# Kernel tuning notes

Hardware: AMD Instinct MI355X
Metric: run time of the kernel (lower is better)

## Reference

```python
import jax, jax.numpy as jnp
import numpy as np

N = 50000      # nodes per type
E = 800000     # edges per relation
CIN = 64       # in_channels
H, O = 2, 32   # heads, out_channels
HID = H * O    # hidden
EC = 16        # edge_channels


def setup_inputs() -> dict:
    key = jax.random.key(0)
    ks = jax.random.split(key, 30)
    f = lambda i, shape, s=0.1: jax.random.normal(ks[i], shape, dtype=jnp.float32) * s
    inp = {
        'x_a': f(0, (N, CIN), 1.0), 'x_b': f(1, (N, CIN), 1.0),
        'edge_attr1': f(2, (E, EC), 1.0), 'edge_attr2': f(3, (E, EC), 1.0),
        'Wq_a': f(4, (CIN, HID)), 'Wk_a': f(5, (CIN, HID)), 'Wv_a': f(6, (CIN, HID)),
        'Wq_b': f(7, (CIN, HID)), 'Wk_b': f(8, (CIN, HID)), 'Wv_b': f(9, (CIN, HID)),
        'emb_a': f(10, (HID,)), 'emb_b': f(11, (HID,)),
        'rel1': f(12, (HID,)), 'rel2': f(13, (HID,)),
        'We': f(14, (EC, HID)), 'a_attn': f(15, (4 * O,)),
        'Wo_a': f(16, (HID, O)), 'bo_a': f(17, (O,)),
        'Wo_b': f(18, (HID, O)), 'bo_b': f(19, (O,)),
        'Wr_a': f(20, (CIN, O)), 'Wr_b': f(21, (CIN, O)),
        'row1': jax.random.randint(ks[22], (E,), 0, N),
        'col1': jax.random.randint(ks[23], (E,), 0, N),
        'row2': jax.random.randint(ks[24], (E,), 0, N),
        'col2': jax.random.randint(ks[25], (E,), 0, N),
    }
    return inp


def _edge_softmax(scores, col, num_dst):
    # softmax over incoming edges of each destination node; scores: [E, H]
    m = jax.ops.segment_max(scores, col, num_segments=num_dst)      # [N, H]
    ex = jnp.exp(scores - m[col])
    s = jax.ops.segment_sum(ex, col, num_segments=num_dst)          # [N, H]
    return ex / s[col]


def _relation(q_dst, k_src, v_src, emb_src, emb_dst, rel_emb, edge_bias,
              row, col, a_attn, num_dst):
    eb = edge_bias                                                  # [E, H, O]
    qd = q_dst[col] + emb_dst.reshape(1, H, O)
    ks = k_src[row] + emb_src.reshape(1, H, O)
    rb = jnp.broadcast_to(rel_emb.reshape(1, H, O), qd.shape)
    attn_in = jnp.concatenate([qd, ks, rb, eb], axis=-1)            # [E, H, 4O]
    scores = jnp.einsum('ehd,d->eh', jnp.tanh(attn_in), a_attn)    # [E, H]
    w = _edge_softmax(scores, col, num_dst)                         # [E, H]
    msg = v_src[row] + rel_emb.reshape(1, H, O) + eb                # [E, H, O]
    agg = jax.ops.segment_sum(msg * w[..., None], col, num_segments=num_dst)
    return agg.reshape(num_dst, H * O)


def reference(x_a, x_b, edge_attr1, edge_attr2,
              Wq_a, Wk_a, Wv_a, Wq_b, Wk_b, Wv_b,
              emb_a, emb_b, rel1, rel2, We, a_attn,
              Wo_a, bo_a, Wo_b, bo_b, Wr_a, Wr_b,
              row1, col1, row2, col2):
    q_a = (x_a @ Wq_a).reshape(-1, H, O)
    k_a = (x_a @ Wk_a).reshape(-1, H, O)
    v_a = (x_a @ Wv_a).reshape(-1, H, O)
    q_b = (x_b @ Wq_b).reshape(-1, H, O)
    k_b = (x_b @ Wk_b).reshape(-1, H, O)
    v_b = (x_b @ Wv_b).reshape(-1, H, O)

    # relation r1: a -> b
    eb1 = (edge_attr1 @ We).reshape(-1, H, O)
    out_b = _relation(q_b, k_a, v_a, emb_a, emb_b, rel1, eb1, row1, col1, a_attn, N)
    # relation r2: b -> a
    eb2 = (edge_attr2 @ We).reshape(-1, H, O)
    out_a = _relation(q_a, k_b, v_b, emb_b, emb_a, rel2, eb2, row2, col2, a_attn, N)

    fin_a = out_a @ Wo_a + bo_a + x_a @ Wr_a                        # [N, O]
    fin_b = out_b @ Wo_b + bo_b + x_b @ Wr_b                        # [N, O]
    return jnp.concatenate([fin_a, fin_b], axis=0)                  # [2N, O]
```

## Files before the change

### kernel.cpp

```cpp
#include <hip/hip_runtime.h>
#include <hip/hip_bf16.h>

typedef __hip_bfloat16 bf16;
typedef __attribute__((ext_vector_type(8))) short short8;
typedef __attribute__((ext_vector_type(4))) float float4v;

static __device__ __forceinline__ float b2f(bf16 x) { return __bfloat162float(x); }

static __device__ __forceinline__ float ldf(const void* p, size_t i, int f32) {
    return f32 ? ((const float*)p)[i] : b2f(((const bf16*)p)[i]);
}
static __device__ __forceinline__ void stf(void* p, size_t i, int f32, float v) {
    if (f32) ((float*)p)[i] = v;
    else     ((bf16*)p)[i] = __float2bfloat16(v);
}
static __device__ __forceinline__ unsigned short f2bf_bits(float f) {
    bf16 h = __float2bfloat16(f);
    return *(unsigned short*)&h;
}

static __device__ __forceinline__ float fast_tanh(float x) {
    float t = __expf(2.f * x);
    return 1.f - 2.f * __builtin_amdgcn_rcpf(t + 1.f);
}

__global__ void detect_kernel(const unsigned short* __restrict__ a, int* __restrict__ flag)
{
    __shared__ int cnt;
    if (threadIdx.x == 0) cnt = 0;
    __syncthreads();
    unsigned e = (a[threadIdx.x] >> 7) & 0xFF;
    if (e < 100 || e > 133) atomicAdd(&cnt, 1);
    __syncthreads();
    if (threadIdx.x == 0) *flag = (cnt >= 16) ? 1 : 0;
}

__global__ __launch_bounds__(256) void prep_small_kernel(
    const void* __restrict__ W0, const void* __restrict__ W1,
    const void* __restrict__ W2, const void* __restrict__ W3,
    const void* __restrict__ W4, const void* __restrict__ W5,
    const void* __restrict__ Wr_a, const void* __restrict__ Wr_b,
    const void* __restrict__ We,
    const void* __restrict__ Wo_a, const void* __restrict__ Wo_b,
    const void* __restrict__ rel1, const void* __restrict__ rel2,
    const void* __restrict__ a_attn, const int* __restrict__ flagp,
    unsigned short* __restrict__ wt,
    float* __restrict__ M1, float* __restrict__ c321,
    float* __restrict__ M2, float* __restrict__ c322,
    float* __restrict__ cvals)
{
    const int f32 = *flagp;
    const int bid = blockIdx.x;
    if (bid < 6) {
        const void* src;
        switch (bid) {
            case 0: src = W0; break; case 1: src = W1; break; case 2: src = W2; break;
            case 3: src = W3; break; case 4: src = W4; break; default: src = W5; break;
        }
        unsigned short* dst = wt + bid * 4096;
        for (int i = threadIdx.x; i < 4096; i += 256) {
            int c = i >> 6, j = i & 63;
            dst[j * 64 + c] = f2bf_bits(ldf(src, c * 64 + j, f32));
        }
    } else if (bid < 8) {
        const void* src = (bid == 6) ? Wr_a : Wr_b;
        unsigned short* dst = wt + 24576 + (bid - 6) * 2048;
        for (int i = threadIdx.x; i < 2048; i += 256) {
            int c = i >> 5, j = i & 31;
            dst[j * 64 + c] = f2bf_bits(ldf(src, c * 32 + j, f32));
        }
    } else if (bid < 10) {
        const int sel = bid - 8;
        const void* Wo  = sel ? Wo_a : Wo_b;
        const void* rel = sel ? rel2 : rel1;
        float* M   = sel ? M2 : M1;
        float* c32 = sel ? c322 : c321;
        const int t = threadIdx.x;
        for (int i = t; i < 1024; i += 256) {
            int m = i >> 5, j = i & 31;
            int h = m >> 4, c = m & 15;
            float s = 0.f;
            for (int jj = 0; jj < 32; ++jj)
                s += ldf(We, c * 64 + h * 32 + jj, f32) * ldf(Wo, (size_t)(h * 32 + jj) * 32 + j, f32);
            M[m * 32 + j] = s;
        }
        if (t < 32) {
            float s2 = 0.f;
            for (int ch = 0; ch < 64; ++ch)
                s2 += ldf(rel, ch, f32) * ldf(Wo, (size_t)ch * 32 + t, f32);
            c32[t] = s2;
        }
        if (t == 252 || t == 253) {
            int h = t - 252;
            float s3 = 0.f;
            for (int l = 0; l < 32; ++l)
                s3 += tanhf(ldf(rel, h * 32 + l, f32)) * ldf(a_attn, 64 + l, f32);
            cvals[sel * 2 + h] = s3;
        }
    } else {
        unsigned short* wet = wt + 28672;
        for (int i = threadIdx.x; i < 1024; i += 256) {
            int n = i >> 4, k = i & 15;
            wet[n * 16 + k] = f2bf_bits(ldf(We, k * 64 + n, f32));
        }
    }
}

__global__ __launch_bounds__(256) void node_prep_mfma_kernel(
    const void* __restrict__ x_a, const void* __restrict__ x_b,
    const unsigned short* __restrict__ wt,
    const void* __restrict__ emb_a, const void* __restrict__ emb_b,
    const void* __restrict__ a_attn, const int* __restrict__ flagp,
    unsigned short* __restrict__ v_a, unsigned short* __restrict__ v_b,
    float* __restrict__ r_a, float* __restrict__ r_b,
    float* __restrict__ sq_a, float* __restrict__ sk_a,
    float* __restrict__ sq_b, float* __restrict__ sk_b,
    int n_nodes, int tiles)
{
    const int f32 = *flagp;
    const int wave_id = blockIdx.x * 4 + (threadIdx.x >> 6);
    if (wave_id >= 2 * tiles) return;
    const int type = (wave_id >= tiles);
    const int tile = type ? (wave_id - tiles) : wave_id;

    const void* xp = type ? x_b : x_a;
    const unsigned short* wq = wt + (type ? 3 * 4096 : 0);
    const unsigned short* wk = wq + 4096;
    const unsigned short* wv = wk + 4096;
    const unsigned short* wr = wt + 24576 + (type ? 2048 : 0);
    const void* embp = type ? emb_b : emb_a;
    unsigned short* v_out = type ? v_b : v_a;
    float*  r_out  = type ? r_b : r_a;
    float2* sq_out = (float2*)(type ? sq_b : sq_a);
    float2* sk_out = (float2*)(type ? sk_b : sk_a);

    const int lane = threadIdx.x & 63;
    const int ml   = lane & 15;
    const int g    = lane >> 4;
    const int g8   = g * 8;

    float embc[4], acq[4], ack[4];
    #pragma unroll
    for (int t = 0; t < 4; ++t) {
        int colt = t * 16 + ml;
        embc[t] = ldf(embp, colt, f32);
        acq[t]  = ldf(a_attn, colt & 31, f32);
        ack[t]  = ldf(a_attn, 32 + (colt & 31), f32);
    }

    short8 Bq[4][2], Bk[4][2], Bv[4][2], Br[2][2];
    #pragma unroll
    for (int t = 0; t < 4; ++t) {
        const int rowo = (t * 16 + ml) * 64;
        #pragma unroll
        for (int kh = 0; kh < 2; ++kh) {
            const int o = rowo + kh * 32 + g8;
            Bq[t][kh] = __builtin_bit_cast(short8, *(const uint4*)(wq + o));
            Bk[t][kh] = __builtin_bit_cast(short8, *(const uint4*)(wk + o));
            Bv[t][kh] = __builtin_bit_cast(short8, *(const uint4*)(wv + o));
            if (t < 2)
                Br[t][kh] = __builtin_bit_cast(short8, *(const uint4*)(wr + o));
        }
    }

    const int n0 = tile << 4;
    int nr = n0 + ml; if (nr > n_nodes - 1) nr = n_nodes - 1;
    short8 A0, A1;
    if (f32) {
        const float4* xr = (const float4*)((const float*)xp + (size_t)nr * 64);
        float4 f0 = xr[2*g], f1 = xr[2*g+1], f2 = xr[8+2*g], f3 = xr[9+2*g];
        short8 a0, a1;
        a0[0]=(short)f2bf_bits(f0.x); a0[1]=(short)f2bf_bits(f0.y);
        a0[2]=(short)f2bf_bits(f0.z); a0[3]=(short)f2bf_bits(f0.w);
        a0[4]=(short)f2bf_bits(f1.x); a0[5]=(short)f2bf_bits(f1.y);
        a0[6]=(short)f2bf_bits(f1.z); a0[7]=(short)f2bf_bits(f1.w);
        a1[0]=(short)f2bf_bits(f2.x); a1[1]=(short)f2bf_bits(f2.y);
        a1[2]=(short)f2bf_bits(f2.z); a1[3]=(short)f2bf_bits(f2.w);
        a1[4]=(short)f2bf_bits(f3.x); a1[5]=(short)f2bf_bits(f3.y);
        a1[6]=(short)f2bf_bits(f3.z); a1[7]=(short)f2bf_bits(f3.w);
        A0 = a0; A1 = a1;
    } else {
        const uint4* xr = (const uint4*)((const bf16*)xp + (size_t)nr * 64);
        A0 = __builtin_bit_cast(short8, xr[g]);
        A1 = __builtin_bit_cast(short8, xr[4 + g]);
    }

    float4v accq[4], acck[4], accv[4], accr[2];
    #pragma unroll
    for (int t = 0; t < 4; ++t) {
        float4v z = {0.f, 0.f, 0.f, 0.f};
        accq[t] = z; acck[t] = z; accv[t] = z;
        if (t < 2) accr[t] = z;
    }
    #pragma unroll
    for (int t = 0; t < 4; ++t) {
        accq[t] = __builtin_amdgcn_mfma_f32_16x16x32_bf16(A0, Bq[t][0], accq[t], 0, 0, 0);
        accq[t] = __builtin_amdgcn_mfma_f32_16x16x32_bf16(A1, Bq[t][1], accq[t], 0, 0, 0);
        acck[t] = __builtin_amdgcn_mfma_f32_16x16x32_bf16(A0, Bk[t][0], acck[t], 0, 0, 0);
        acck[t] = __builtin_amdgcn_mfma_f32_16x16x32_bf16(A1, Bk[t][1], acck[t], 0, 0, 0);
        accv[t] = __builtin_amdgcn_mfma_f32_16x16x32_bf16(A0, Bv[t][0], accv[t], 0, 0, 0);
        accv[t] = __builtin_amdgcn_mfma_f32_16x16x32_bf16(A1, Bv[t][1], accv[t], 0, 0, 0);
        if (t < 2) {
            accr[t] = __builtin_amdgcn_mfma_f32_16x16x32_bf16(A0, Br[t][0], accr[t], 0, 0, 0);
            accr[t] = __builtin_amdgcn_mfma_f32_16x16x32_bf16(A1, Br[t][1], accr[t], 0, 0, 0);
        }
    }

    #pragma unroll
    for (int t = 0; t < 4; ++t) {
        #pragma unroll
        for (int r = 0; r < 4; ++r) {
            int node = n0 + g * 4 + r;
            if (node < n_nodes) {
                v_out[(size_t)node * 64 + t * 16 + ml] = f2bf_bits(accv[t][r]);
                if (t < 2) r_out[(size_t)node * 32 + t * 16 + ml] = accr[t][r];
            }
        }
    }

    #pragma unroll
    for (int r = 0; r < 4; ++r) {
        float q0 = fast_tanh(accq[0][r] + embc[0]) * acq[0]
                 + fast_tanh(accq[1][r] + embc[1]) * acq[1];
        float q1 = fast_tanh(accq[2][r] + embc[2]) * acq[2]
                 + fast_tanh(accq[3][r] + embc[3]) * acq[3];
        float k0 = fast_tanh(acck[0][r] + embc[0]) * ack[0]
                 + fast_tanh(acck[1][r] + embc[1]) * ack[1];
        float k1 = fast_tanh(acck[2][r] + embc[2]) * ack[2]
                 + fast_tanh(acck[3][r] + embc[3]) * ack[3];
        #pragma unroll
        for (int o = 1; o < 16; o <<= 1) {
            q0 += __shfl_xor(q0, o, 64); q1 += __shfl_xor(q1, o, 64);
            k0 += __shfl_xor(k0, o, 64); k1 += __shfl_xor(k1, o, 64);
        }
        int node = n0 + g * 4 + r;
        if (ml == 0 && node < n_nodes) {
            sq_out[node] = make_float2(q0, q1);
            sk_out[node] = make_float2(k0, k1);
        }
    }
}

__global__ __launch_bounds__(256) void hist_kernel(
    const int* __restrict__ col1, const int* __restrict__ col2,
    int* __restrict__ cnt, int n_nodes, int num_e)
{
    const int sel = blockIdx.x & 1;
    const int bx  = blockIdx.x >> 1;
    const int* col = sel ? col2 : col1;
    const int rb = sel ? n_nodes : 0;
    int e = bx * 256 + threadIdx.x;
    if (e < num_e) atomicAdd(&cnt[rb + col[e]], 1);
}

__global__ __launch_bounds__(256) void scan1_kernel(const int* __restrict__ cnt,
                                                    int* __restrict__ partial, int n)
{
    __shared__ int wsum[4];
    int t = threadIdx.x;
    int i0 = blockIdx.x * 512 + 2 * t;
    int s = ((i0 < n) ? cnt[i0] : 0) + ((i0 + 1 < n) ? cnt[i0 + 1] : 0);
    #pragma unroll
    for (int o = 32; o; o >>= 1) s += __shfl_xor(s, o, 64);
    if ((t & 63) == 0) wsum[t >> 6] = s;
    __syncthreads();
    if (t == 0) partial[blockIdx.x] = wsum[0] + wsum[1] + wsum[2] + wsum[3];
}

__global__ void scan2_kernel(const int* __restrict__ partial, int* __restrict__ pp,
                             int* __restrict__ off, int nch, int noff)
{
    int lane = threadIdx.x;
    int running = 0;
    for (int base = 0; base < nch; base += 64) {
        int i = base + lane;
        int o = (i < nch) ? partial[i] : 0;
        int v = o;
        #pragma unroll
        for (int d = 1; d < 64; d <<= 1) {
            int u = __shfl_up(v, d, 64);
            if (lane >= d) v += u;
        }
        if (i < nch) pp[i] = running + v - o;
        running += __shfl(v, 63, 64);
    }
    if (lane == 0) off[noff] = running;
}

__global__ __launch_bounds__(256) void scan3_kernel(const int* __restrict__ cnt,
                                                    const int* __restrict__ pp,
                                                    int* __restrict__ off,
                                                    int* __restrict__ cursor, int n)
{
    __shared__ int tmp[256];
    int t = threadIdx.x;
    int i0 = blockIdx.x * 512 + 2 * t;
    int v0 = (i0 < n) ? cnt[i0] : 0;
    int v1 = (i0 + 1 < n) ? cnt[i0 + 1] : 0;
    int pair = v0 + v1;
    tmp[t] = pair;
    __syncthreads();
    for (int d = 1; d < 256; d <<= 1) {
        int x = (t >= d) ? tmp[t - d] : 0;
        __syncthreads();
        tmp[t] += x;
        __syncthreads();
    }
    int excl = tmp[t] - pair + pp[blockIdx.x];
    if (i0 < n)     { off[i0] = excl;          cursor[i0] = excl; }
    if (i0 + 1 < n) { off[i0 + 1] = excl + v0; cursor[i0 + 1] = excl + v0; }
}

__global__ __launch_bounds__(256) void edge_score_scatter_kernel(
    const void* __restrict__ ea1p, const void* __restrict__ ea2p,
    const unsigned short* __restrict__ wet,
    const int* __restrict__ row1, const int* __restrict__ col1,
    const int* __restrict__ row2, const int* __restrict__ col2,
    const float* __restrict__ sq_bp, const float* __restrict__ sk_ap,
    const float* __restrict__ sq_ap, const float* __restrict__ sk_bp,
    const float* __restrict__ cvals, const void* __restrict__ a_attn,
    const int* __restrict__ flagp, int* __restrict__ cursor,
    uint4* __restrict__ payload, int n_nodes, int num_e)
{
    const int f32 = *flagp;
    const int sel = blockIdx.x & 1;
    const int bx  = blockIdx.x >> 1;
    const void* ea = sel ? ea2p : ea1p;
    const int* row = sel ? row2 : row1;
    const int* col = sel ? col2 : col1;
    const float* sq_dst = sel ? sq_ap : sq_bp;
    const float* sk_src = sel ? sk_bp : sk_ap;
    const int rb = sel ? n_nodes : 0;

    const int lane = threadIdx.x & 63;
    const int wv   = threadIdx.x >> 6;
    const int ml   = lane & 15;
    const int g    = lane >> 4;
    const int rsel = lane & 3;

    const int base = bx * 512 + wv * 128;
    if (base >= num_e) return;

    const short8 zero8 = {0, 0, 0, 0, 0, 0, 0, 0};

    short8 B[4];
    #pragma unroll
    for (int t = 0; t < 4; ++t)
        B[t] = (g < 2) ? __builtin_bit_cast(short8, *(const uint4*)(wet + (t * 16 + ml) * 16 + g * 8))
                       : zero8;
    float av[4];
    #pragma unroll
    for (int t = 0; t < 4; ++t) av[t] = ldf(a_attn, 96 + ((t * 16 + ml) & 31), f32);
    const float c0 = cvals[sel * 2 + 0];
    const float c1 = cvals[sel * 2 + 1];

    short8 A[8];
    #pragma unroll
    for (int it = 0; it < 8; ++it) {
        int ec = base + it * 16 + ml; if (ec > num_e - 1) ec = num_e - 1;
        if (g < 2) {
            if (f32) {
                const float4* p = (const float4*)((const float*)ea + (size_t)ec * 16 + g * 8);
                float4 f0 = p[0], f1 = p[1];
                short8 a;
                a[0] = (short)f2bf_bits(f0.x); a[1] = (short)f2bf_bits(f0.y);
                a[2] = (short)f2bf_bits(f0.z); a[3] = (short)f2bf_bits(f0.w);
                a[4] = (short)f2bf_bits(f1.x); a[5] = (short)f2bf_bits(f1.y);
                a[6] = (short)f2bf_bits(f1.z); a[7] = (short)f2bf_bits(f1.w);
                A[it] = a;
            } else {
                A[it] = __builtin_bit_cast(short8, *(const uint4*)((const bf16*)ea + (size_t)ec * 16 + g * 8));
            }
        } else {
            A[it] = zero8;
        }
    }

    int ppos[8]; unsigned psrc[8]; float2 psq[8], psk[8];
    #pragma unroll
    for (int it = 0; it < 8; ++it) {
        ppos[it] = 0; psrc[it] = 0;
        psq[it] = make_float2(0.f, 0.f); psk[it] = make_float2(0.f, 0.f);
    }
    if (ml < 4) {
        int pcol[8];
        #pragma unroll
        for (int it = 0; it < 8; ++it) {
            int e = base + it * 16 + g * 4 + rsel;
            int ec = (e < num_e) ? e : (num_e - 1);
            pcol[it] = col[ec];
            psrc[it] = (unsigned)row[ec];
        }
        #pragma unroll
        for (int it = 0; it < 8; ++it) {
            psq[it] = ((const float2*)sq_dst)[pcol[it]];
            psk[it] = ((const float2*)sk_src)[psrc[it]];
        }
        #pragma unroll
        for (int it = 0; it < 8; ++it) {
            int e = base + it * 16 + g * 4 + rsel;
            ppos[it] = (e < num_e) ? atomicAdd(&cursor[rb + pcol[it]], 1) : 0;
        }
    }

    #pragma unroll
    for (int it = 0; it < 8; ++it) {
        const int e0 = base + it * 16;
        if (e0 < num_e) {
            float4v z = {0.f, 0.f, 0.f, 0.f};
            float4v acc0 = z, acc1 = z, acc2 = z, acc3 = z;
            acc0 = __builtin_amdgcn_mfma_f32_16x16x32_bf16(A[it], B[0], acc0, 0, 0, 0);
            acc1 = __builtin_amdgcn_mfma_f32_16x16x32_bf16(A[it], B[1], acc1, 0, 0, 0);
            acc2 = __builtin_amdgcn_mfma_f32_16x16x32_bf16(A[it], B[2], acc2, 0, 0, 0);
            acc3 = __builtin_amdgcn_mfma_f32_16x16x32_bf16(A[it], B[3], acc3, 0, 0, 0);

            float s0[4], s1[4];
            #pragma unroll
            for (int r = 0; r < 4; ++r) {
                s0[r] = fast_tanh(acc0[r]) * av[0] + fast_tanh(acc1[r]) * av[1];
                s1[r] = fast_tanh(acc2[r]) * av[2] + fast_tanh(acc3[r]) * av[3];
            }
            #pragma unroll
            for (int o = 1; o < 16; o <<= 1) {
                #pragma unroll
                for (int r = 0; r < 4; ++r) {
                    s0[r] += __shfl_xor(s0[r], o, 64);
                    s1[r] += __shfl_xor(s1[r], o, 64);
                }
            }

            const bool fin = (ml < 4) && (e0 + g * 4 + rsel < num_e);
            if (fin) {
                float a0 = (rsel == 0) ? s0[0] : (rsel == 1) ? s0[1] : (rsel == 2) ? s0[2] : s0[3];
                float a1 = (rsel == 0) ? s1[0] : (rsel == 1) ? s1[1] : (rsel == 2) ? s1[2] : s1[3];
                float v0 = fminf(30.f, fmaxf(-30.f, a0 + psq[it].x + psk[it].x + c0));
                float v1 = fminf(30.f, fmaxf(-30.f, a1 + psq[it].y + psk[it].y + c1));
                uint4* rec = payload + (size_t)3 * ppos[it];
                rec[0] = make_uint4(psrc[it], __float_as_uint(__expf(v0)),
                                    __float_as_uint(__expf(v1)), 0u);
            }
            const int srcl = ((lane & 12) << 2) | (lane & 3);
            const int posx = __shfl(ppos[it], srcl, 64);
            if (lane < 32 && (e0 + ml < num_e)) {
                uint4* rec = payload + (size_t)3 * posx;
                rec[1 + g] = __builtin_bit_cast(uint4, A[it]);
            }
        }
    }
}

__global__ __launch_bounds__(256) void agg_final_kernel(
    const uint4* __restrict__ payload, const int* __restrict__ off,
    const unsigned short* __restrict__ v_a, const unsigned short* __restrict__ v_b,
    const float* __restrict__ r_a, const float* __restrict__ r_b,
    const void* __restrict__ Wo_a, const void* __restrict__ Wo_b,
    const void* __restrict__ bo_a, const void* __restrict__ bo_b,
    const float* __restrict__ M1, const float* __restrict__ M2,
    const float* __restrict__ c321, const float* __restrict__ c322,
    const int* __restrict__ flagp, void* __restrict__ out,
    int n_nodes, int nbh)
{
    const int sel = blockIdx.x & 1;
    const int bx  = blockIdx.x >> 1;
    const unsigned short* v_src = sel ? v_b : v_a;
    const float* r_src = sel ? r_a : r_b;
    const void*  Wo    = sel ? Wo_a : Wo_b;
    const void*  bo    = sel ? bo_a : bo_b;
    const float* M     = sel ? M2 : M1;
    const float* c32   = sel ? c322 : c321;
    const int relbase  = sel ? n_nodes : 0;
    const size_t out_off = sel ? 0 : (size_t)n_nodes * 32;

    const int f32  = *flagp;
    const int lane = threadIdx.x & 63;
    const int wv   = threadIdx.x >> 6;
    const int j    = lane & 31;
    const int half = lane >> 5;
    const int c16  = lane & 15;
    const bool hi  = (lane >= 32);

    __shared__ float stage[4][96];

    float WoR[32], MR[16];
    const int cb = half * 32;
    #pragma unroll
    for (int cc = 0; cc < 32; ++cc)
        WoR[cc] = ldf(Wo, (size_t)(cb + cc) * 32 + j, f32);
    const int ub = half * 16;
    #pragma unroll
    for (int cc = 0; cc < 16; ++cc) MR[cc] = M[(ub + cc) * 32 + j];
    const float boR  = ldf(bo, j, f32);
    const float c32R = c32[j];

    const int stride = nbh * 4;
    const int iters  = (n_nodes + stride - 1) / stride;
    int d = bx * 4 + wv;

    for (int it = 0; it < iters; ++it, d += stride) {
        const bool valid = (d < n_nodes);
        const int dd  = valid ? d : (n_nodes - 1);
        const int idx = relbase + dd;
        const int b   = __builtin_amdgcn_readfirstlane(off[idx]);
        const int en  = __builtin_amdgcn_readfirstlane(off[idx + 1]);
        const int deg = en - b;

        const float rv = r_src[(size_t)dd * 32 + j];

        float den0 = 0.f, den1 = 0.f, y = 0.f, ua = 0.f;
        int k = b;
        #pragma unroll 1
        for (; k + 8 <= en; k += 8) {
            uint4 m[8];
            #pragma unroll
            for (int q = 0; q < 8; ++q) m[q] = payload[(size_t)3 * (k + q)];
            float ev[8];
            #pragma unroll
            for (int q = 0; q < 8; ++q) {
                const unsigned short* pq = (const unsigned short*)(payload + (size_t)3 * (k + q) + 1);
                ev[q] = __uint_as_float((unsigned)pq[c16] << 16);
            }
            float vv[8];
            #pragma unroll
            for (int q = 0; q < 8; ++q)
                vv[q] = __uint_as_float((unsigned)v_src[(size_t)m[q].x * 64 + lane] << 16);
            #pragma unroll
            for (int q = 0; q < 8; ++q) {
                float e0 = __uint_as_float(m[q].y), e1 = __uint_as_float(m[q].z);
                den0 += e0; den1 += e1;
                float xw = hi ? e1 : e0;
                y  = fmaf(xw, vv[q], y);
                ua = fmaf(xw, ev[q], ua);
            }
        }
        #pragma unroll 1
        for (; k < en; ++k) {
            uint4 mm = payload[(size_t)3 * k];
            const unsigned short* pq = (const unsigned short*)(payload + (size_t)3 * k + 1);
            float evs = __uint_as_float((unsigned)pq[c16] << 16);
            float vvs = __uint_as_float((unsigned)v_src[(size_t)mm.x * 64 + lane] << 16);
            float e0 = __uint_as_float(mm.y), e1 = __uint_as_float(mm.z);
            den0 += e0; den1 += e1;
            float xw = hi ? e1 : e0;
            y  = fmaf(xw, vvs, y);
            ua = fmaf(xw, evs, ua);
        }

        float inv0 = (deg > 0) ? __builtin_amdgcn_rcpf(den0) : 0.f;
        float inv1 = (deg > 0) ? __builtin_amdgcn_rcpf(den1) : 0.f;
        const float invh = hi ? inv1 : inv0;
        y  *= invh;
        ua *= invh;

        float* st = stage[wv];
        st[lane] = y;
        if ((lane & 31) < 16) st[64 + half * 16 + c16] = ua;
        __asm__ volatile("s_waitcnt lgkmcnt(0)" ::: "memory");

        float acc = 0.f;
        #pragma unroll
        for (int cc = 0; cc < 32; ++cc)
            acc = fmaf(st[cb + cc], WoR[cc], acc);
        #pragma unroll
        for (int cc = 0; cc < 16; ++cc)
            acc = fmaf(st[64 + ub + cc], MR[cc], acc);

        float other = __shfl(acc, lane ^ 32, 64);
        if (valid && lane < 32) {
            float o = acc + other + boR + rv + ((deg > 0) ? c32R : 0.f);
            stf(out, out_off + (size_t)dd * 32 + j, f32, o);
        }
        __asm__ volatile("" ::: "memory");
        __builtin_amdgcn_wave_barrier();
    }
}

extern "C" void kernel_launch(void* const* d_in, const int* in_sizes, int n_in,
                              void* d_out, int out_size, void* d_ws, size_t ws_size,
                              hipStream_t stream)
{
    const void* x_a   = d_in[0];
    const void* x_b   = d_in[1];
    const void* ea1   = d_in[2];
    const void* ea2   = d_in[3];
    const void* Wq_a  = d_in[4];
    const void* Wk_a  = d_in[5];
    const void* Wv_a  = d_in[6];
    const void* Wq_b  = d_in[7];
    const void* Wk_b  = d_in[8];
    const void* Wv_b  = d_in[9];
    const void* emb_a = d_in[10];
    const void* emb_b = d_in[11];
    const void* rel1  = d_in[12];
    const void* rel2  = d_in[13];
    const void* We    = d_in[14];
    const void* a_at  = d_in[15];
    const void* Wo_a  = d_in[16];
    const void* bo_a  = d_in[17];
    const void* Wo_b  = d_in[18];
    const void* bo_b  = d_in[19];
    const void* Wr_a  = d_in[20];
    const void* Wr_b  = d_in[21];
    const int*  row1  = (const int*)d_in[22];
    const int*  col1  = (const int*)d_in[23];
    const int*  row2  = (const int*)d_in[24];
    const int*  col2  = (const int*)d_in[25];

    const int N = in_sizes[0] / 64;
    const int E = in_sizes[22];

    float* ws = (float*)d_ws;
    size_t off = 0;
    int*   flag = (int*)ws;        off += 64;
    unsigned short* v_a = (unsigned short*)(ws + off); off += (size_t)N * 32;
    unsigned short* v_b = (unsigned short*)(ws + off); off += (size_t)N * 32;
    float* r_a  = ws + off;        off += (size_t)N * 32;
    float* r_b  = ws + off;        off += (size_t)N * 32;
    float* sq_a = ws + off;        off += (size_t)N * 2;
    float* sk_a = ws + off;        off += (size_t)N * 2;
    float* sq_b = ws + off;        off += (size_t)N * 2;
    float* sk_b = ws + off;        off += (size_t)N * 2;
    float* cvals = ws + off;       off += 4;
    off = (off + 3) & ~(size_t)3;
    unsigned short* wt = (unsigned short*)(ws + off); off += 29696 / 2;
    float* M1   = ws + off;        off += 1024;
    float* c321 = ws + off;        off += 32;
    float* M2   = ws + off;        off += 1024;
    float* c322 = ws + off;        off += 32;
    int*   cnt    = (int*)(ws + off);  off += (size_t)2 * N;
    int*   offs   = (int*)(ws + off);  off += (size_t)2 * N + 2;
    int*   cursor = (int*)(ws + off);  off += (size_t)2 * N;
    int*   partial = (int*)(ws + off); off += 512;
    int*   pp      = (int*)(ws + off); off += 512;
    off = (off + 3) & ~(size_t)3;
    uint4* payload = (uint4*)(ws + off); off += (size_t)2 * E * 12;

    const int tiles        = (N + 15) >> 4;
    const int mfma_blocks  = (2 * tiles + 3) / 4;
    const int score_blocks = (E + 511) / 512;
    const int eb_blocks    = (E + 255) / 256;
    const int nch          = (2 * N + 511) / 512;
    const int agg_half     = 2048;

    detect_kernel<<<1, 128, 0, stream>>>((const unsigned short*)a_at, flag);
    hipMemsetAsync(cnt, 0, (size_t)2 * N * sizeof(int), stream);

    prep_small_kernel<<<11, 256, 0, stream>>>(
        Wq_a, Wk_a, Wv_a, Wq_b, Wk_b, Wv_b, Wr_a, Wr_b,
        We, Wo_a, Wo_b, rel1, rel2, a_at, flag,
        wt, M1, c321, M2, c322, cvals);

    node_prep_mfma_kernel<<<mfma_blocks, 256, 0, stream>>>(
        x_a, x_b, wt, emb_a, emb_b, a_at, flag,
        v_a, v_b, r_a, r_b, sq_a, sk_a, sq_b, sk_b, N, tiles);

    hist_kernel<<<2 * eb_blocks, 256, 0, stream>>>(col1, col2, cnt, N, E);
    scan1_kernel<<<nch, 256, 0, stream>>>(cnt, partial, 2 * N);
    scan2_kernel<<<1, 64, 0, stream>>>(partial, pp, offs, nch, 2 * N);
    scan3_kernel<<<nch, 256, 0, stream>>>(cnt, pp, offs, cursor, 2 * N);

    edge_score_scatter_kernel<<<2 * score_blocks, 256, 0, stream>>>(
        ea1, ea2, wt + 28672, row1, col1, row2, col2,
        sq_b, sk_a, sq_a, sk_b, cvals, a_at, flag,
        cursor, payload, N, E);

    agg_final_kernel<<<2 * agg_half, 256, 0, stream>>>(
        payload, offs, v_a, v_b, r_a, r_b, Wo_a, Wo_b, bo_a, bo_b,
        M1, M2, c321, c322, flag, d_out, N, agg_half);
}
```

Measured before the change: 542.1 us.

## Fuse histogram into node-prep launch, halve edge-score tile, prefetch agg offsets

The degree histogram blocks are appended to the node-prep MFMA launch, which removes one kernel launch and lets the atomics overlap with node projection work. The edge score/scatter kernel now handles 64 edges per wave instead of 128, which doubles the number of blocks and cuts register pressure. The aggregation loop software-prefetches the next destination's CSR offsets and residual value to hide load latency. In exchange, the node-prep kernel carries a larger grid with divergent block roles, and the per-edge weight setup is spread over more waves.

```diff
diff --git a/kernel.cpp b/kernel.cpp
--- a/kernel.cpp
+++ b/kernel.cpp
@@ -115,9 +115,23 @@
     float* __restrict__ r_a, float* __restrict__ r_b,
     float* __restrict__ sq_a, float* __restrict__ sk_a,
     float* __restrict__ sq_b, float* __restrict__ sk_b,
-    int n_nodes, int tiles)
+    const int* __restrict__ col1, const int* __restrict__ col2,
+    int* __restrict__ cnt,
+    int n_nodes, int tiles, int mfma_blocks, int num_e)
 {
     const int f32 = *flagp;
+
+    if ((int)blockIdx.x >= mfma_blocks) {
+        const int hb  = blockIdx.x - mfma_blocks;
+        const int sel = hb & 1;
+        const int bx  = hb >> 1;
+        const int* col = sel ? col2 : col1;
+        const int rb = sel ? n_nodes : 0;
+        int e = bx * 256 + threadIdx.x;
+        if (e < num_e) atomicAdd(&cnt[rb + col[e]], 1);
+        return;
+    }
+
     const int wave_id = blockIdx.x * 4 + (threadIdx.x >> 6);
     if (wave_id >= 2 * tiles) return;
     const int type = (wave_id >= tiles);
@@ -241,18 +255,6 @@
     }
 }
 
-__global__ __launch_bounds__(256) void hist_kernel(
-    const int* __restrict__ col1, const int* __restrict__ col2,
-    int* __restrict__ cnt, int n_nodes, int num_e)
-{
-    const int sel = blockIdx.x & 1;
-    const int bx  = blockIdx.x >> 1;
-    const int* col = sel ? col2 : col1;
-    const int rb = sel ? n_nodes : 0;
-    int e = bx * 256 + threadIdx.x;
-    if (e < num_e) atomicAdd(&cnt[rb + col[e]], 1);
-}
-
 __global__ __launch_bounds__(256) void scan1_kernel(const int* __restrict__ cnt,
                                                     int* __restrict__ partial, int n)
 {
@@ -338,7 +340,7 @@
     const int g    = lane >> 4;
     const int rsel = lane & 3;
 
-    const int base = bx * 512 + wv * 128;
+    const int base = bx * 256 + wv * 64;
     if (base >= num_e) return;
 
     const short8 zero8 = {0, 0, 0, 0, 0, 0, 0, 0};
@@ -354,9 +356,9 @@
     const float c0 = cvals[sel * 2 + 0];
     const float c1 = cvals[sel * 2 + 1];
 
-    short8 A[8];
-    #pragma unroll
-    for (int it = 0; it < 8; ++it) {
+    short8 A[4];
+    #pragma unroll
+    for (int it = 0; it < 4; ++it) {
         int ec = base + it * 16 + ml; if (ec > num_e - 1) ec = num_e - 1;
         if (g < 2) {
             if (f32) {
@@ -376,35 +378,35 @@
         }
     }
 
-    int ppos[8]; unsigned psrc[8]; float2 psq[8], psk[8];
-    #pragma unroll
-    for (int it = 0; it < 8; ++it) {
+    int ppos[4]; unsigned psrc[4]; float2 psq[4], psk[4];
+    #pragma unroll
+    for (int it = 0; it < 4; ++it) {
         ppos[it] = 0; psrc[it] = 0;
         psq[it] = make_float2(0.f, 0.f); psk[it] = make_float2(0.f, 0.f);
     }
     if (ml < 4) {
-        int pcol[8];
-        #pragma unroll
-        for (int it = 0; it < 8; ++it) {
+        int pcol[4];
+        #pragma unroll
+        for (int it = 0; it < 4; ++it) {
             int e = base + it * 16 + g * 4 + rsel;
             int ec = (e < num_e) ? e : (num_e - 1);
             pcol[it] = col[ec];
             psrc[it] = (unsigned)row[ec];
         }
         #pragma unroll
-        for (int it = 0; it < 8; ++it) {
+        for (int it = 0; it < 4; ++it) {
             psq[it] = ((const float2*)sq_dst)[pcol[it]];
             psk[it] = ((const float2*)sk_src)[psrc[it]];
         }
         #pragma unroll
-        for (int it = 0; it < 8; ++it) {
+        for (int it = 0; it < 4; ++it) {
             int e = base + it * 16 + g * 4 + rsel;
             ppos[it] = (e < num_e) ? atomicAdd(&cursor[rb + pcol[it]], 1) : 0;
         }
     }
 
     #pragma unroll
-    for (int it = 0; it < 8; ++it) {
+    for (int it = 0; it < 4; ++it) {
         const int e0 = base + it * 16;
         if (e0 < num_e) {
             float4v z = {0.f, 0.f, 0.f, 0.f};
@@ -496,15 +498,28 @@
     const int iters  = (n_nodes + stride - 1) / stride;
     int d = bx * 4 + wv;
 
+    int dd0 = (d < n_nodes) ? d : (n_nodes - 1);
+    int b_c  = off[relbase + dd0];
+    int en_c = off[relbase + dd0 + 1];
+    float rv_c = r_src[(size_t)dd0 * 32 + j];
+
     for (int it = 0; it < iters; ++it, d += stride) {
         const bool valid = (d < n_nodes);
         const int dd  = valid ? d : (n_nodes - 1);
-        const int idx = relbase + dd;
-        const int b   = __builtin_amdgcn_readfirstlane(off[idx]);
-        const int en  = __builtin_amdgcn_readfirstlane(off[idx + 1]);
+
+        int b_n = 0, en_n = 0; float rv_n = 0.f;
+        if (it + 1 < iters) {
+            int dn  = d + stride;
+            int ddn = (dn < n_nodes) ? dn : (n_nodes - 1);
+            b_n  = off[relbase + ddn];
+            en_n = off[relbase + ddn + 1];
+            rv_n = r_src[(size_t)ddn * 32 + j];
+        }
+
+        const int b   = __builtin_amdgcn_readfirstlane(b_c);
+        const int en  = __builtin_amdgcn_readfirstlane(en_c);
         const int deg = en - b;
-
-        const float rv = r_src[(size_t)dd * 32 + j];
+        const float rv = rv_c;
 
         float den0 = 0.f, den1 = 0.f, y = 0.f, ua = 0.f;
         int k = b;
@@ -571,6 +586,8 @@
         }
         __asm__ volatile("" ::: "memory");
         __builtin_amdgcn_wave_barrier();
+
+        b_c = b_n; en_c = en_n; rv_c = rv_n;
     }
 }
 
@@ -636,8 +653,8 @@
 
     const int tiles        = (N + 15) >> 4;
     const int mfma_blocks  = (2 * tiles + 3) / 4;
-    const int score_blocks = (E + 511) / 512;
     const int eb_blocks    = (E + 255) / 256;
+    const int score_blocks = (E + 255) / 256;
     const int nch          = (2 * N + 511) / 512;
     const int agg_half     = 2048;
 
@@ -649,11 +666,11 @@
         We, Wo_a, Wo_b, rel1, rel2, a_at, flag,
         wt, M1, c321, M2, c322, cvals);
 
-    node_prep_mfma_kernel<<<mfma_blocks, 256, 0, stream>>>(
+    node_prep_mfma_kernel<<<mfma_blocks + 2 * eb_blocks, 256, 0, stream>>>(
         x_a, x_b, wt, emb_a, emb_b, a_at, flag,
-        v_a, v_b, r_a, r_b, sq_a, sk_a, sq_b, sk_b, N, tiles);
-
-    hist_kernel<<<2 * eb_blocks, 256, 0, stream>>>(col1, col2, cnt, N, E);
+        v_a, v_b, r_a, r_b, sq_a, sk_a, sq_b, sk_b,
+        col1, col2, cnt, N, tiles, mfma_blocks, E);
+
     scan1_kernel<<<nch, 256, 0, stream>>>(cnt, partial, 2 * N);
     scan2_kernel<<<1, 64, 0, stream>>>(partial, pp, offs, nch, 2 * N);
     scan3_kernel<<<nch, 256, 0, stream>>>(cnt, pp, offs, cursor, 2 * N);
```

Result: faster. 525.3 us (-3.1%).
